# Kernel tuning notes

Measured on AMD Instinct MI355X. Metric: run time of the kernel, lower is better.

Reference implementation:

```python
import jax, jax.numpy as jnp
import numpy as np

N_NODES = 100000
N_EDGES = 1600000
F_IN = 100
HEADS = 3
HEAD_DIM = 64
HIDDEN = HEADS * HEAD_DIM  # 192
NUM_GRAPHS = 128
NUM_CLASSES = 2
NEG_SLOPE_ATT = 0.2   # PyG GATConv attention leaky_relu slope
NEG_SLOPE_ACT = 0.01  # F.leaky_relu default slope


def setup_inputs() -> dict:
    key = jax.random.key(0)
    ks = jax.random.split(key, 9)
    x = jax.random.normal(ks[0], (N_NODES, F_IN), dtype=jnp.float32)
    edge_index = jax.random.randint(ks[1], (2, N_EDGES), 0, N_NODES, dtype=jnp.int64)
    batch = jnp.sort(jax.random.randint(ks[2], (N_NODES,), 0, NUM_GRAPHS, dtype=jnp.int64))
    s = 0.05
    W = jax.random.normal(ks[3], (F_IN, HIDDEN), dtype=jnp.float32) * s
    att_src = jax.random.normal(ks[4], (HEADS, HEAD_DIM), dtype=jnp.float32) * s
    att_dst = jax.random.normal(ks[5], (HEADS, HEAD_DIM), dtype=jnp.float32) * s
    bias = jax.random.normal(ks[6], (HIDDEN,), dtype=jnp.float32) * s
    cls_W = jax.random.normal(ks[7], (HIDDEN, NUM_CLASSES), dtype=jnp.float32) * s
    cls_b = jax.random.normal(ks[8], (NUM_CLASSES,), dtype=jnp.float32) * s
    return {"x": x, "edge_index": edge_index, "batch": batch, "W": W,
            "att_src": att_src, "att_dst": att_dst, "bias": bias,
            "cls_W": cls_W, "cls_b": cls_b}


def _gat_forward(x, edge_index, batch, W, att_src, att_dst, bias, cls_W, cls_b):
    N = x.shape[0]
    # PyG GATConv adds self-loops by default
    loops = jnp.arange(N, dtype=edge_index.dtype)
    src = jnp.concatenate([edge_index[0], loops])
    dst = jnp.concatenate([edge_index[1], loops])

    h = (x @ W).reshape(N, HEADS, HEAD_DIM)          # [N,H,C]
    a_src = jnp.sum(h * att_src, axis=-1)            # [N,H]
    a_dst = jnp.sum(h * att_dst, axis=-1)            # [N,H]

    e = a_src[src] + a_dst[dst]                      # [Etot,H]
    e = jax.nn.leaky_relu(e, NEG_SLOPE_ATT)

    # segment softmax over incoming edges of each destination node
    m = jax.ops.segment_max(e, dst, num_segments=N)  # [N,H]
    e = jnp.exp(e - m[dst])
    denom = jax.ops.segment_sum(e, dst, num_segments=N)
    alpha = e / denom[dst]                           # [Etot,H]

    msg = h[src] * alpha[:, :, None]                 # [Etot,H,C]
    out = jax.ops.segment_sum(msg, dst, num_segments=N).reshape(N, HIDDEN) + bias

    out = jax.nn.leaky_relu(out, NEG_SLOPE_ACT)      # F.leaky_relu (dropout inactive: eval)
    pooled = jax.ops.segment_max(out, batch, num_segments=NUM_GRAPHS)  # global_max_pool
    return pooled @ cls_W + cls_b                    # [NUM_GRAPHS, NUM_CLASSES]


def reference(x, edge_index, batch, W, att_src, att_dst, bias, cls_W, cls_b):
    return _gat_forward(x, edge_index, batch, W, att_src, att_dst, bias, cls_W, cls_b)
```

## Files before the change

kernel.cpp:

```cpp
#include <hip/hip_runtime.h>
#include <math.h>

#define N_NODES   100000
#define N_EDGES   1600000
#define ETOT      1700000
#define F_IN      100
#define HEADS     3
#define HEAD_DIM  64
#define HIDDEN    192
#define NUM_GRAPHS 128
#define NUM_CLASSES 2
#define SLAB      64
#define WT_COLS   208
#define KPAD      128
#define NCHUNK    ((ETOT + 1023) / 1024)
#define DRANGE    (N_NODES / 8)
#define NGEMM     (N_NODES / 32)
#define OSTRIDE   200
#define GAGG      8
#define CAP       64

typedef unsigned short ushort_t;
typedef __attribute__((ext_vector_type(8))) short short8;
typedef __attribute__((ext_vector_type(4))) float floatx4;

__device__ __forceinline__ unsigned f2ord(float f) {
    unsigned u = __float_as_uint(f);
    return (u & 0x80000000u) ? ~u : (u | 0x80000000u);
}
__device__ __forceinline__ float ord2f(unsigned u) {
    return __uint_as_float((u & 0x80000000u) ? (u & 0x7fffffffu) : ~u);
}
__device__ __forceinline__ unsigned bf16rn(float f) {
    unsigned u = __float_as_uint(f);
    return (u + 0x7fffu + ((u >> 16) & 1u)) >> 16;
}

__global__ __launch_bounds__(256) void k_prep(
        const float* __restrict__ W, const float* __restrict__ att_src,
        const float* __restrict__ att_dst,
        ushort_t* __restrict__ WT_hi, ushort_t* __restrict__ WT_lo) {
    const int c0 = blockIdx.x * 8;
    const int t = threadIdx.x;
    __shared__ float wsv_s[F_IN * 6];
    if (c0 < HIDDEN + 6 && c0 + 8 > HIDDEN) {
        for (int p = t; p < F_IN * 6; p += 256) {
            int k = p / 6, j = p % 6;
            const float* a = (j < 3) ? att_src : att_dst;
            int hh = j % 3;
            float s = 0.f;
            for (int c = 0; c < HEAD_DIM; c++)
                s += W[k * HIDDEN + hh * HEAD_DIM + c] * a[hh * HEAD_DIM + c];
            wsv_s[p] = s;
        }
        __syncthreads();
    }
    for (int idx = t; idx < 8 * KPAD; idx += 256) {
        int col = c0 + (idx >> 7), k = idx & (KPAD - 1);
        float v = 0.f;
        if (k < F_IN) {
            if (col < HIDDEN) v = W[k * HIDDEN + col];
            else if (col < HIDDEN + 6) v = wsv_s[k * 6 + (col - HIDDEN)];
        }
        unsigned hi = bf16rn(v);
        WT_hi[col * KPAD + k] = (ushort_t)hi;
        float lo = v - __uint_as_float(hi << 16);
        WT_lo[col * KPAD + k] = (ushort_t)bf16rn(lo);
    }
}

__global__ __launch_bounds__(256) void k_mega(
        const float* __restrict__ x,
        const ushort_t* __restrict__ WT_hi, const ushort_t* __restrict__ WT_lo,
        ushort_t* __restrict__ hb,
        float* __restrict__ asrc, float* __restrict__ adst,
        const int* __restrict__ ei, int* __restrict__ count,
        int* __restrict__ srcs) {
    __shared__ ushort_t lds[32 * 136 * 2];
    const int tid = threadIdx.x;

    if (blockIdx.x >= NGEMM) {
        const int cls = blockIdx.x & 7;
        const int chunk = (blockIdx.x - NGEMM) >> 3;
        const int dlo = cls * DRANGE, dhi = dlo + DRANGE;
        const int base = chunk * 1024 + tid;
#pragma unroll
        for (int q = 0; q < 4; q++) {
            int j = base + q * 256;
            if (j >= ETOT) continue;
            int d = (j < N_EDGES) ? ei[N_EDGES + j] : (j - N_EDGES);
            int s = (j < N_EDGES) ? ei[j] : d;
            if (d < dlo || d >= dhi) continue;
            int pos = atomicAdd(&count[d], 1);
            if (pos < CAP) srcs[d * CAP + pos] = s;
        }
        return;
    }

    ushort_t* xs_hi = lds;
    ushort_t* xs_lo = lds + 32 * 136;
    const int base = blockIdx.x * 32;
    for (int idx = tid; idx < 32 * KPAD; idx += 256) {
        int row = idx >> 7, k = idx & (KPAD - 1);
        float v = (k < F_IN) ? x[(base + row) * F_IN + k] : 0.f;
        unsigned hi = bf16rn(v);
        xs_hi[row * 136 + k] = (ushort_t)hi;
        float lo = v - __uint_as_float(hi << 16);
        xs_lo[row * 136 + k] = (ushort_t)bf16rn(lo);
    }
    __syncthreads();

    const int wid = tid >> 6, l = tid & 63;
    const int row16 = l & 15, g = l >> 4;
    const int NT = (wid == 3) ? 4 : 3;
    const int t0 = wid * 3;

    floatx4 acc[2][4];
#pragma unroll
    for (int m = 0; m < 2; m++)
#pragma unroll
        for (int i = 0; i < 4; i++) acc[m][i] = (floatx4)0.f;

#pragma unroll
    for (int c = 0; c < 4; c++) {
        const int ke = g * 8 + c * 32;
        short8 ah0 = *(const short8*)(xs_hi + row16 * 136 + ke);
        short8 al0 = *(const short8*)(xs_lo + row16 * 136 + ke);
        short8 ah1 = *(const short8*)(xs_hi + (16 + row16) * 136 + ke);
        short8 al1 = *(const short8*)(xs_lo + (16 + row16) * 136 + ke);
#pragma unroll
        for (int ti = 0; ti < 4; ti++) {
            if (ti >= NT) break;
            const int col = (t0 + ti) * 16 + row16;
            short8 bh = *(const short8*)(WT_hi + col * KPAD + ke);
            short8 bl = *(const short8*)(WT_lo + col * KPAD + ke);
            acc[0][ti] = __builtin_amdgcn_mfma_f32_16x16x32_bf16(ah0, bh, acc[0][ti], 0, 0, 0);
            acc[0][ti] = __builtin_amdgcn_mfma_f32_16x16x32_bf16(ah0, bl, acc[0][ti], 0, 0, 0);
            acc[0][ti] = __builtin_amdgcn_mfma_f32_16x16x32_bf16(al0, bh, acc[0][ti], 0, 0, 0);
            acc[1][ti] = __builtin_amdgcn_mfma_f32_16x16x32_bf16(ah1, bh, acc[1][ti], 0, 0, 0);
            acc[1][ti] = __builtin_amdgcn_mfma_f32_16x16x32_bf16(ah1, bl, acc[1][ti], 0, 0, 0);
            acc[1][ti] = __builtin_amdgcn_mfma_f32_16x16x32_bf16(al1, bh, acc[1][ti], 0, 0, 0);
        }
    }

    __syncthreads();

#pragma unroll
    for (int ti = 0; ti < 4; ti++) {
        if (ti >= NT) break;
        const int tile = t0 + ti;
        if (tile < 12) {
#pragma unroll
            for (int m = 0; m < 2; m++)
#pragma unroll
                for (int r = 0; r < 4; r++) {
                    int node = m * 16 + g * 4 + r;
                    lds[node * OSTRIDE + tile * 16 + row16] =
                        (ushort_t)bf16rn(acc[m][ti][r]);
                }
        } else if (row16 < 6) {
#pragma unroll
            for (int m = 0; m < 2; m++)
#pragma unroll
                for (int r = 0; r < 4; r++) {
                    int node = base + m * 16 + g * 4 + r;
                    if (row16 < 3) asrc[node * HEADS + row16] = acc[m][ti][r];
                    else           adst[node * HEADS + (row16 - 3)] = acc[m][ti][r];
                }
        }
    }
    __syncthreads();

    uint4* hb4 = (uint4*)(hb + (size_t)base * HIDDEN);
#pragma unroll
    for (int i = 0; i < 3; i++) {
        int q = tid + i * 256;
        int row = q / 24, c8 = q % 24;
        hb4[q] = *(const uint4*)(lds + row * OSTRIDE + c8 * 8);
    }
}

__global__ __launch_bounds__(192) void k_aggr(const int* __restrict__ count,
        const int* __restrict__ srcs, const float* __restrict__ asrc,
        const float* __restrict__ adst, const ushort_t* __restrict__ hb,
        const float* __restrict__ bias, ushort_t* __restrict__ ob, int nbase) {
    const int n0 = nbase + blockIdx.x * GAGG;
    const int tid = threadIdx.x;
    const int head = tid >> 6, lane = tid & 63;
    const char* hbase = (const char*)hb + head * 128 + (lane & 7) * 16;
    const int src0 = lane >> 3;

    int cntv = (lane < GAGG) ? count[n0 + lane] : 0;
    float adv = (lane < GAGG * HEADS) ? adst[n0 * HEADS + lane] : 0.f;
    float bv[8];
    {
        const int c0 = head * HEAD_DIM + (lane & 7) * 8;
#pragma unroll
        for (int k = 0; k < 8; k++) bv[k] = bias[c0 + k];
    }

    for (int g = 0; g < GAGG; g++) {
        const int cnt = __shfl(cntv, g);
        const float ad = __shfl(adv, g * HEADS + head);
        const int n = n0 + g;

        int s = srcs[n * CAP + lane];
        float myexp = 0.f; int myoff = 0;
        if (lane < cnt) {
            float e = asrc[s * HEADS + head] + ad;
            e = (e > 0.f) ? e : 0.2f * e;
            myexp = expf(e);
            myoff = s * (HIDDEN * 2);
        }

        float dsum = myexp;
#pragma unroll
        for (int m = 1; m < 64; m <<= 1) dsum += __shfl_xor(dsum, m);

        float acc[8];
#pragma unroll
        for (int k = 0; k < 8; k++) acc[k] = 0.f;
        int groups = (cnt + 7) >> 3;
#pragma unroll 2
        for (int j = 0; j < groups; j++) {
            int sl = j * 8 + src0;
            float a   = __shfl(myexp, sl);
            int   off = __shfl(myoff, sl);
            uint4 u = *(const uint4*)(hbase + off);
            acc[0] += a * __uint_as_float(u.x << 16);
            acc[1] += a * __uint_as_float(u.x & 0xffff0000u);
            acc[2] += a * __uint_as_float(u.y << 16);
            acc[3] += a * __uint_as_float(u.y & 0xffff0000u);
            acc[4] += a * __uint_as_float(u.z << 16);
            acc[5] += a * __uint_as_float(u.z & 0xffff0000u);
            acc[6] += a * __uint_as_float(u.w << 16);
            acc[7] += a * __uint_as_float(u.w & 0xffff0000u);
        }

#pragma unroll
        for (int k = 0; k < 8; k++) {
            acc[k] += __shfl_xor(acc[k], 8);
            acc[k] += __shfl_xor(acc[k], 16);
            acc[k] += __shfl_xor(acc[k], 32);
        }

        if (lane < 8) {
            const float inv = 1.f / dsum;
            const int c0 = head * HEAD_DIM + lane * 8;
            unsigned pk[4];
#pragma unroll
            for (int q = 0; q < 4; q++) {
                float v0 = acc[2 * q] * inv + bv[2 * q];
                float v1 = acc[2 * q + 1] * inv + bv[2 * q + 1];
                v0 = (v0 > 0.f) ? v0 : 0.01f * v0;
                v1 = (v1 > 0.f) ? v1 : 0.01f * v1;
                pk[q] = bf16rn(v0) | (bf16rn(v1) << 16);
            }
            *(uint4*)(ob + n * HIDDEN + c0) = make_uint4(pk[0], pk[1], pk[2], pk[3]);
        }
    }
}

__global__ __launch_bounds__(192) void k_pool(
        const ushort_t* __restrict__ ob, const int* __restrict__ batch,
        unsigned* __restrict__ pooled) {
    const int t = threadIdx.x;
    const int n0 = blockIdx.x * SLAB;
    int n1 = n0 + SLAB; if (n1 > N_NODES) n1 = N_NODES;
    int curg = batch[n0];
    float m = -INFINITY;
    for (int n = n0; n < n1; n++) {
        int g = batch[n];
        if (g != curg) {
            atomicMax(&pooled[curg * HIDDEN + t], f2ord(m));
            m = -INFINITY; curg = g;
        }
        m = fmaxf(m, __uint_as_float((unsigned)ob[n * HIDDEN + t] << 16));
    }
    atomicMax(&pooled[curg * HIDDEN + t], f2ord(m));
}

__global__ __launch_bounds__(64) void k_cls(const unsigned* __restrict__ pooled,
        const float* __restrict__ clsW, const float* __restrict__ clsb,
        float* __restrict__ out) {
    const int g = blockIdx.x, lane = threadIdx.x;
    float s0 = 0.f, s1 = 0.f;
#pragma unroll
    for (int i = 0; i < 3; i++) {
        int f = i * 64 + lane;
        float pv = ord2f(pooled[g * HIDDEN + f]);
        s0 += pv * clsW[f * NUM_CLASSES];
        s1 += pv * clsW[f * NUM_CLASSES + 1];
    }
#pragma unroll
    for (int m = 1; m < 64; m <<= 1) {
        s0 += __shfl_xor(s0, m);
        s1 += __shfl_xor(s1, m);
    }
    if (lane == 0) {
        out[g * NUM_CLASSES]     = s0 + clsb[0];
        out[g * NUM_CLASSES + 1] = s1 + clsb[1];
    }
}

extern "C" void kernel_launch(void* const* d_in, const int* in_sizes, int n_in,
                              void* d_out, int out_size, void* d_ws, size_t ws_size,
                              hipStream_t stream) {
    const float* x       = (const float*)d_in[0];
    const int*   ei      = (const int*)d_in[1];
    const int*   batch   = (const int*)d_in[2];
    const float* W       = (const float*)d_in[3];
    const float* att_src = (const float*)d_in[4];
    const float* att_dst = (const float*)d_in[5];
    const float* bias    = (const float*)d_in[6];
    const float* clsW    = (const float*)d_in[7];
    const float* clsb    = (const float*)d_in[8];
    float* out = (float*)d_out;

    char* p = (char*)d_ws;
    auto alloc = [&](size_t bytes) {
        char* r = p; p += (bytes + 255) & ~size_t(255); return r;
    };
    ushort_t* hb     = (ushort_t*)alloc(sizeof(ushort_t) * N_NODES * HIDDEN);
    ushort_t* ob     = (ushort_t*)alloc(sizeof(ushort_t) * N_NODES * HIDDEN);
    float*    asrc   = (float*)   alloc(sizeof(float) * N_NODES * HEADS);
    float*    adst   = (float*)   alloc(sizeof(float) * N_NODES * HEADS);
    int*      count  = (int*)     alloc(sizeof(int) * N_NODES);
    int*      srcs   = (int*)     alloc(sizeof(int) * (size_t)N_NODES * CAP);
    ushort_t* WT_hi  = (ushort_t*)alloc(sizeof(ushort_t) * WT_COLS * KPAD);
    ushort_t* WT_lo  = (ushort_t*)alloc(sizeof(ushort_t) * WT_COLS * KPAD);
    unsigned* pooled = (unsigned*)alloc(sizeof(unsigned) * NUM_GRAPHS * HIDDEN);

    hipMemsetAsync(count, 0, sizeof(int) * N_NODES, stream);
    hipMemsetAsync(pooled, 0, sizeof(unsigned) * NUM_GRAPHS * HIDDEN, stream);

    k_prep<<<WT_COLS / 8, 256, 0, stream>>>(W, att_src, att_dst, WT_hi, WT_lo);
    k_mega<<<NGEMM + NCHUNK * 8, 256, 0, stream>>>(x, WT_hi, WT_lo, hb, asrc, adst,
                                                   ei, count, srcs);
    k_aggr<<<N_NODES / GAGG / 2, 192, 0, stream>>>(count, srcs, asrc, adst, hb, bias, ob, 0);
    k_aggr<<<N_NODES / GAGG / 2, 192, 0, stream>>>(count, srcs, asrc, adst, hb, bias, ob, N_NODES / 2);
    k_pool<<<(N_NODES + SLAB - 1) / SLAB, 192, 0, stream>>>(ob, batch, pooled);
    k_cls<<<NUM_GRAPHS, 64, 0, stream>>>(pooled, clsW, clsb, out);
}
```

Before: 399.7 us.

## Fuse global max pooling into aggregation kernel and drop output buffer

The aggregation kernel now keeps a running per-graph max of the activated outputs in registers and flushes it to the pooled array through shared memory and atomicMax whenever the graph id changes. This removes the bf16 node-output buffer write, the separate pooling kernel and one launch. GAGG is doubled to 16 and the two half-launches are merged into one. The edge-bucketing loop is also split so all edge loads are issued before the atomics, and cnt is clamped to CAP. The cost is extra __syncthreads inside the node loop at graph boundaries.

```diff
diff --git a/kernel.cpp b/kernel.cpp
--- a/kernel.cpp
+++ b/kernel.cpp
@@ -10,14 +10,13 @@
 #define HIDDEN    192
 #define NUM_GRAPHS 128
 #define NUM_CLASSES 2
-#define SLAB      64
 #define WT_COLS   208
 #define KPAD      128
 #define NCHUNK    ((ETOT + 1023) / 1024)
 #define DRANGE    (N_NODES / 8)
 #define NGEMM     (N_NODES / 32)
 #define OSTRIDE   200
-#define GAGG      8
+#define GAGG      16
 #define CAP       64
 
 typedef unsigned short ushort_t;
@@ -84,15 +83,20 @@
         const int chunk = (blockIdx.x - NGEMM) >> 3;
         const int dlo = cls * DRANGE, dhi = dlo + DRANGE;
         const int base = chunk * 1024 + tid;
+        int d4[4], s4[4];
 #pragma unroll
         for (int q = 0; q < 4; q++) {
             int j = base + q * 256;
-            if (j >= ETOT) continue;
-            int d = (j < N_EDGES) ? ei[N_EDGES + j] : (j - N_EDGES);
-            int s = (j < N_EDGES) ? ei[j] : d;
+            if (j >= ETOT) { d4[q] = -1; s4[q] = 0; continue; }
+            d4[q] = (j < N_EDGES) ? ei[N_EDGES + j] : (j - N_EDGES);
+            s4[q] = (j < N_EDGES) ? ei[j] : d4[q];
+        }
+#pragma unroll
+        for (int q = 0; q < 4; q++) {
+            int d = d4[q];
             if (d < dlo || d >= dhi) continue;
             int pos = atomicAdd(&count[d], 1);
-            if (pos < CAP) srcs[d * CAP + pos] = s;
+            if (pos < CAP) srcs[d * CAP + pos] = s4[q];
         }
         return;
     }
@@ -183,24 +187,45 @@
 __global__ __launch_bounds__(192) void k_aggr(const int* __restrict__ count,
         const int* __restrict__ srcs, const float* __restrict__ asrc,
         const float* __restrict__ adst, const ushort_t* __restrict__ hb,
-        const float* __restrict__ bias, ushort_t* __restrict__ ob, int nbase) {
-    const int n0 = nbase + blockIdx.x * GAGG;
+        const float* __restrict__ bias, const int* __restrict__ batch,
+        unsigned* __restrict__ pooled) {
+    __shared__ float sm[HIDDEN];
+    const int n0 = blockIdx.x * GAGG;
     const int tid = threadIdx.x;
     const int head = tid >> 6, lane = tid & 63;
     const char* hbase = (const char*)hb + head * 128 + (lane & 7) * 16;
     const int src0 = lane >> 3;
+    const int c0 = head * HEAD_DIM + (lane & 7) * 8;
 
     int cntv = (lane < GAGG) ? count[n0 + lane] : 0;
+    int bgv  = (lane < GAGG) ? batch[n0 + lane] : 0;
     float adv = (lane < GAGG * HEADS) ? adst[n0 * HEADS + lane] : 0.f;
     float bv[8];
-    {
-        const int c0 = head * HEAD_DIM + (lane & 7) * 8;
-#pragma unroll
-        for (int k = 0; k < 8; k++) bv[k] = bias[c0 + k];
-    }
+#pragma unroll
+    for (int k = 0; k < 8; k++) bv[k] = bias[c0 + k];
+
+    float vmax[8];
+#pragma unroll
+    for (int k = 0; k < 8; k++) vmax[k] = -INFINITY;
+    int curg = __shfl(bgv, 0);
 
     for (int g = 0; g < GAGG; g++) {
-        const int cnt = __shfl(cntv, g);
+        const int gg = __shfl(bgv, g);
+        if (gg != curg) {
+            if (lane < 8) {
+#pragma unroll
+                for (int k = 0; k < 8; k++) sm[c0 + k] = vmax[k];
+            }
+            __syncthreads();
+            atomicMax(&pooled[curg * HIDDEN + tid], f2ord(sm[tid]));
+            __syncthreads();
+#pragma unroll
+            for (int k = 0; k < 8; k++) vmax[k] = -INFINITY;
+            curg = gg;
+        }
+
+        int cnt = __shfl(cntv, g);
+        if (cnt > CAP) cnt = CAP;
         const float ad = __shfl(adv, g * HEADS + head);
         const int n = n0 + g;
 
@@ -246,38 +271,21 @@
 
         if (lane < 8) {
             const float inv = 1.f / dsum;
-            const int c0 = head * HEAD_DIM + lane * 8;
-            unsigned pk[4];
-#pragma unroll
-            for (int q = 0; q < 4; q++) {
-                float v0 = acc[2 * q] * inv + bv[2 * q];
-                float v1 = acc[2 * q + 1] * inv + bv[2 * q + 1];
-                v0 = (v0 > 0.f) ? v0 : 0.01f * v0;
-                v1 = (v1 > 0.f) ? v1 : 0.01f * v1;
-                pk[q] = bf16rn(v0) | (bf16rn(v1) << 16);
+#pragma unroll
+            for (int k = 0; k < 8; k++) {
+                float v = acc[k] * inv + bv[k];
+                v = (v > 0.f) ? v : 0.01f * v;
+                vmax[k] = fmaxf(vmax[k], v);
             }
-            *(uint4*)(ob + n * HIDDEN + c0) = make_uint4(pk[0], pk[1], pk[2], pk[3]);
-        }
-    }
-}
-
-__global__ __launch_bounds__(192) void k_pool(
-        const ushort_t* __restrict__ ob, const int* __restrict__ batch,
-        unsigned* __restrict__ pooled) {
-    const int t = threadIdx.x;
-    const int n0 = blockIdx.x * SLAB;
-    int n1 = n0 + SLAB; if (n1 > N_NODES) n1 = N_NODES;
-    int curg = batch[n0];
-    float m = -INFINITY;
-    for (int n = n0; n < n1; n++) {
-        int g = batch[n];
-        if (g != curg) {
-            atomicMax(&pooled[curg * HIDDEN + t], f2ord(m));
-            m = -INFINITY; curg = g;
-        }
-        m = fmaxf(m, __uint_as_float((unsigned)ob[n * HIDDEN + t] << 16));
-    }
-    atomicMax(&pooled[curg * HIDDEN + t], f2ord(m));
+        }
+    }
+
+    if (lane < 8) {
+#pragma unroll
+        for (int k = 0; k < 8; k++) sm[c0 + k] = vmax[k];
+    }
+    __syncthreads();
+    atomicMax(&pooled[curg * HIDDEN + tid], f2ord(sm[tid]));
 }
 
 __global__ __launch_bounds__(64) void k_cls(const unsigned* __restrict__ pooled,
@@ -322,7 +330,6 @@
         char* r = p; p += (bytes + 255) & ~size_t(255); return r;
     };
     ushort_t* hb     = (ushort_t*)alloc(sizeof(ushort_t) * N_NODES * HIDDEN);
-    ushort_t* ob     = (ushort_t*)alloc(sizeof(ushort_t) * N_NODES * HIDDEN);
     float*    asrc   = (float*)   alloc(sizeof(float) * N_NODES * HEADS);
     float*    adst   = (float*)   alloc(sizeof(float) * N_NODES * HEADS);
     int*      count  = (int*)     alloc(sizeof(int) * N_NODES);
@@ -337,8 +344,7 @@
     k_prep<<<WT_COLS / 8, 256, 0, stream>>>(W, att_src, att_dst, WT_hi, WT_lo);
     k_mega<<<NGEMM + NCHUNK * 8, 256, 0, stream>>>(x, WT_hi, WT_lo, hb, asrc, adst,
                                                    ei, count, srcs);
-    k_aggr<<<N_NODES / GAGG / 2, 192, 0, stream>>>(count, srcs, asrc, adst, hb, bias, ob, 0);
-    k_aggr<<<N_NODES / GAGG / 2, 192, 0, stream>>>(count, srcs, asrc, adst, hb, bias, ob, N_NODES / 2);
-    k_pool<<<(N_NODES + SLAB - 1) / SLAB, 192, 0, stream>>>(ob, batch, pooled);
+    k_aggr<<<N_NODES / GAGG, 192, 0, stream>>>(count, srcs, asrc, adst, hb, bias,
+                                               batch, pooled);
     k_cls<<<NUM_GRAPHS, 64, 0, stream>>>(pooled, clsW, clsb, out);
 }
```

Result: faster. 372.7 us (-6.8%).
